# Performance work log

Measured on AMD Instinct MI355X. Metric: run time of the kernel, lower is better.

Reference implementation:

```python
import jax, jax.numpy as jnp
import numpy as np

DELTA = 0.1
PAD = 2  # kernel_size // 2


def _step(x, W):
    # circular padding then VALID 5x5 cross-correlation (matches torch Conv2d circular)
    xp = jnp.pad(x, ((0, 0), (0, 0), (PAD, PAD), (PAD, PAD)), mode='wrap')
    y = jax.lax.conv_general_dilated(
        xp, W, window_strides=(1, 1), padding='VALID',
        dimension_numbers=('NCHW', 'OIHW', 'NCHW'))
    return jnp.clip(x + DELTA * jax.nn.relu(y), 0.0, 1.0)


def setup_inputs() -> dict:
    key = jax.random.key(0)
    k1, k2 = jax.random.split(key)
    x = jax.random.uniform(k1, (16, 3, 1024, 1024), dtype=jnp.float32)
    W = jax.random.normal(k2, (3, 3, 5, 5), dtype=jnp.float32) * 0.2
    return {"x": x, "W": W, "steps": 10}


def reference(x, W, steps):
    for _ in range(steps):
        x = _step(x, W)
    return x
```

## Files before the change

### kernel.cpp

```cpp
#include <hip/hip_runtime.h>


#define HH 1024
#define WW 1024
#define CC 3
#define NB 16
#define TW 128
#define TH 16
#define LW 132
#define LH 20
#define DELTA 0.1f

__global__ __launch_bounds__(256)
void ca_step(const float* __restrict__ src, float* __restrict__ dst,
             const float* __restrict__ Wg) {
    __shared__ float tile[CC][LH][LW];
    __shared__ float wsm[CC * 5 * 16];

    const int tid = threadIdx.x;
    const int w0 = blockIdx.x * TW;
    const int h0 = blockIdx.y * TH;
    const int n  = blockIdx.z;
    const float* srcn = src + (size_t)n * CC * HH * WW;

    if (tid < CC * CC * 25) {
        int oc = tid / 75;
        int rem = tid - oc * 75;
        int ic = rem / 25;
        int r2 = rem - ic * 25;
        int kh = r2 / 5;
        int kw = r2 - kh * 5;
        wsm[(ic * 5 + kh) * 16 + oc * 5 + kw] = Wg[tid];
    }

    for (int f = tid; f < CC * LH * 32; f += 256) {
        int c   = f / (LH * 32);
        int rem = f - c * (LH * 32);
        int row = rem >> 5;
        int c4  = rem & 31;
        int gh = (h0 + row - 2) & (HH - 1);
        const float4 v = *(const float4*)&srcn[((size_t)c * HH + gh) * WW + w0 + 4 * c4];
        float* t = &tile[c][row][2 + 4 * c4];
        *(float2*)&t[0] = make_float2(v.x, v.y);
        *(float2*)&t[2] = make_float2(v.z, v.w);
    }
    if (tid < CC * LH * 2) {
        int side = tid & 1;
        int rf   = tid >> 1;
        int c    = rf / LH;
        int row  = rf - c * LH;
        int gh = (h0 + row - 2) & (HH - 1);
        int gw = side ? ((w0 + TW) & (WW - 1)) : ((w0 - 2) & (WW - 1));
        const float2 v = *(const float2*)&srcn[((size_t)c * HH + gh) * WW + gw];
        *(float2*)&tile[c][row][side ? (2 + TW) : 0] = v;
    }
    __syncthreads();

    const int tx = tid & 31;
    const int ty = tid >> 5;
    const int xb = 4 * tx;

    float acc[2][CC][4];
#pragma unroll
    for (int rg = 0; rg < 2; ++rg)
#pragma unroll
        for (int oc = 0; oc < CC; ++oc)
#pragma unroll
            for (int j = 0; j < 4; ++j) acc[rg][oc][j] = 0.f;
    float xv[2][CC][4];

#pragma unroll
    for (int ic = 0; ic < CC; ++ic) {
#pragma unroll
        for (int kh = 0; kh < 5; ++kh) {
            const float* wrow = &wsm[(ic * 5 + kh) * 16];
            const float4 wA = *(const float4*)&wrow[0];
            const float4 wB = *(const float4*)&wrow[4];
            const float4 wC = *(const float4*)&wrow[8];
            const float4 wD = *(const float4*)&wrow[12];
            const float w_[15] = {wA.x, wA.y, wA.z, wA.w,
                                  wB.x, wB.y, wB.z, wB.w,
                                  wC.x, wC.y, wC.z, wC.w,
                                  wD.x, wD.y, wD.z};
            const float* ra = &tile[ic][ty + kh][xb];
            const float* rb = &tile[ic][ty + 8 + kh][xb];
            float va[8], vb[8];
            *(float4*)&va[0] = *(const float4*)&ra[0];
            *(float4*)&va[4] = *(const float4*)&ra[4];
            *(float4*)&vb[0] = *(const float4*)&rb[0];
            *(float4*)&vb[4] = *(const float4*)&rb[4];
            if (kh == 2) {
#pragma unroll
                for (int j = 0; j < 4; ++j) {
                    xv[0][ic][j] = va[2 + j];
                    xv[1][ic][j] = vb[2 + j];
                }
            }
#pragma unroll
            for (int oc = 0; oc < CC; ++oc) {
#pragma unroll
                for (int kw = 0; kw < 5; ++kw) {
                    const float wv = w_[oc * 5 + kw];
#pragma unroll
                    for (int j = 0; j < 4; ++j) {
                        acc[0][oc][j] = fmaf(va[kw + j], wv, acc[0][oc][j]);
                        acc[1][oc][j] = fmaf(vb[kw + j], wv, acc[1][oc][j]);
                    }
                }
            }
        }
    }

    float* dstn = dst + (size_t)n * CC * HH * WW;
#pragma unroll
    for (int rg = 0; rg < 2; ++rg) {
        const int h = h0 + ty + rg * 8;
#pragma unroll
        for (int oc = 0; oc < CC; ++oc) {
            float4 o;
            o.x = fminf(fmaxf(xv[rg][oc][0] + DELTA * fmaxf(acc[rg][oc][0], 0.f), 0.f), 1.f);
            o.y = fminf(fmaxf(xv[rg][oc][1] + DELTA * fmaxf(acc[rg][oc][1], 0.f), 0.f), 1.f);
            o.z = fminf(fmaxf(xv[rg][oc][2] + DELTA * fmaxf(acc[rg][oc][2], 0.f), 0.f), 1.f);
            o.w = fminf(fmaxf(xv[rg][oc][3] + DELTA * fmaxf(acc[rg][oc][3], 0.f), 0.f), 1.f);
            *(float4*)&dstn[((size_t)oc * HH + h) * WW + w0 + xb] = o;
        }
    }
}

extern "C" void kernel_launch(void* const* d_in, const int* in_sizes, int n_in,
                              void* d_out, int out_size, void* d_ws, size_t ws_size,
                              hipStream_t stream) {
    (void)in_sizes; (void)n_in; (void)out_size;
    const float* x  = (const float*)d_in[0];
    const float* Wg = (const float*)d_in[1];
    const int STEPS = 10;
    float* out = (float*)d_out;
    const size_t buf_bytes = (size_t)NB * CC * HH * WW * sizeof(float);

    dim3 grid(WW / TW, HH / TH, NB);
    dim3 block(256);

    if (ws_size >= buf_bytes) {
        float* tmp = (float*)d_ws;
        const float* s = x;
        for (int i = 1; i <= STEPS; ++i) {
            float* d = (i & 1) ? tmp : out;
            ca_step<<<grid, block, 0, stream>>>(s, d, Wg);
            s = d;
        }
    } else {
        float* tmp = (float*)d_in[0];
        const float* s = x;
        for (int i = 1; i <= STEPS; ++i) {
            float* d = (i & 1) ? out : tmp;
            ca_step<<<grid, block, 0, stream>>>(s, d, Wg);
            s = d;
        }
        hipMemcpyAsync(out, tmp, buf_bytes, hipMemcpyDeviceToDevice, stream);
    }
}
```

Baseline: 1.512 ms.

## Register-block four output rows per thread with rolling row buffer

The block shrinks to 128 threads and each thread now computes four consecutive output rows. Input rows are kept in a rotating four-row register buffer, so each shared-memory row is loaded once per thread instead of once per filter tap row. Weights are read straight from global memory (uniform loads) instead of being staged in shared memory, and the residual x is reread from the tile at the end. This cuts LDS traffic per FMA, at the cost of higher register pressure, fewer threads per tile, and scalar global weight loads inside the inner loop.

```diff
diff --git a/kernel.cpp b/kernel.cpp
--- a/kernel.cpp
+++ b/kernel.cpp
@@ -11,11 +11,10 @@
 #define LH 20
 #define DELTA 0.1f
 
-__global__ __launch_bounds__(256)
+__global__ __launch_bounds__(128, 3)
 void ca_step(const float* __restrict__ src, float* __restrict__ dst,
              const float* __restrict__ Wg) {
     __shared__ float tile[CC][LH][LW];
-    __shared__ float wsm[CC * 5 * 16];
 
     const int tid = threadIdx.x;
     const int w0 = blockIdx.x * TW;
@@ -23,106 +22,95 @@
     const int n  = blockIdx.z;
     const float* srcn = src + (size_t)n * CC * HH * WW;
 
-    if (tid < CC * CC * 25) {
-        int oc = tid / 75;
-        int rem = tid - oc * 75;
-        int ic = rem / 25;
-        int r2 = rem - ic * 25;
-        int kh = r2 / 5;
-        int kw = r2 - kh * 5;
-        wsm[(ic * 5 + kh) * 16 + oc * 5 + kw] = Wg[tid];
-    }
-
-    for (int f = tid; f < CC * LH * 32; f += 256) {
-        int c   = f / (LH * 32);
-        int rem = f - c * (LH * 32);
-        int row = rem >> 5;
-        int c4  = rem & 31;
-        int gh = (h0 + row - 2) & (HH - 1);
+    const int r0 = tid >> 5;
+    const int c4 = tid & 31;
+#pragma unroll
+    for (int k = 0; k < 15; ++k) {
+        const int c     = k / 5;
+        const int strip = k - c * 5;
+        const int row   = strip * 4 + r0;
+        const int gh = (h0 + row - 2) & (HH - 1);
         const float4 v = *(const float4*)&srcn[((size_t)c * HH + gh) * WW + w0 + 4 * c4];
         float* t = &tile[c][row][2 + 4 * c4];
         *(float2*)&t[0] = make_float2(v.x, v.y);
         *(float2*)&t[2] = make_float2(v.z, v.w);
     }
     if (tid < CC * LH * 2) {
-        int side = tid & 1;
-        int rf   = tid >> 1;
-        int c    = rf / LH;
-        int row  = rf - c * LH;
-        int gh = (h0 + row - 2) & (HH - 1);
-        int gw = side ? ((w0 + TW) & (WW - 1)) : ((w0 - 2) & (WW - 1));
+        const int side = tid & 1;
+        const int rf   = tid >> 1;
+        const int c    = rf / LH;
+        const int row  = rf - c * LH;
+        const int gh = (h0 + row - 2) & (HH - 1);
+        const int gw = side ? ((w0 + TW) & (WW - 1)) : ((w0 - 2) & (WW - 1));
         const float2 v = *(const float2*)&srcn[((size_t)c * HH + gh) * WW + gw];
         *(float2*)&tile[c][row][side ? (2 + TW) : 0] = v;
     }
     __syncthreads();
 
-    const int tx = tid & 31;
-    const int ty = tid >> 5;
-    const int xb = 4 * tx;
+    const int tx  = tid & 31;
+    const int ty4 = (tid >> 5) << 2;
+    const int xb  = 4 * tx;
 
-    float acc[2][CC][4];
+    float acc[4][CC][4];
 #pragma unroll
-    for (int rg = 0; rg < 2; ++rg)
+    for (int o = 0; o < 4; ++o)
 #pragma unroll
         for (int oc = 0; oc < CC; ++oc)
 #pragma unroll
-            for (int j = 0; j < 4; ++j) acc[rg][oc][j] = 0.f;
-    float xv[2][CC][4];
+            for (int j = 0; j < 4; ++j) acc[o][oc][j] = 0.f;
 
 #pragma unroll
     for (int ic = 0; ic < CC; ++ic) {
+        float rw[4][8];
+#pragma unroll
+        for (int r = 0; r < 4; ++r) {
+            const float* rp = &tile[ic][ty4 + r][xb];
+            *(float4*)&rw[r][0] = *(const float4*)&rp[0];
+            *(float4*)&rw[r][4] = *(const float4*)&rp[4];
+        }
 #pragma unroll
         for (int kh = 0; kh < 5; ++kh) {
-            const float* wrow = &wsm[(ic * 5 + kh) * 16];
-            const float4 wA = *(const float4*)&wrow[0];
-            const float4 wB = *(const float4*)&wrow[4];
-            const float4 wC = *(const float4*)&wrow[8];
-            const float4 wD = *(const float4*)&wrow[12];
-            const float w_[15] = {wA.x, wA.y, wA.z, wA.w,
-                                  wB.x, wB.y, wB.z, wB.w,
-                                  wC.x, wC.y, wC.z, wC.w,
-                                  wD.x, wD.y, wD.z};
-            const float* ra = &tile[ic][ty + kh][xb];
-            const float* rb = &tile[ic][ty + 8 + kh][xb];
-            float va[8], vb[8];
-            *(float4*)&va[0] = *(const float4*)&ra[0];
-            *(float4*)&va[4] = *(const float4*)&ra[4];
-            *(float4*)&vb[0] = *(const float4*)&rb[0];
-            *(float4*)&vb[4] = *(const float4*)&rb[4];
-            if (kh == 2) {
+            float wsc[CC][5];
 #pragma unroll
-                for (int j = 0; j < 4; ++j) {
-                    xv[0][ic][j] = va[2 + j];
-                    xv[1][ic][j] = vb[2 + j];
-                }
+            for (int oc = 0; oc < CC; ++oc)
+#pragma unroll
+                for (int kw = 0; kw < 5; ++kw)
+                    wsc[oc][kw] = Wg[((oc * CC + ic) * 5 + kh) * 5 + kw];
+#pragma unroll
+            for (int o = 0; o < 4; ++o) {
+#pragma unroll
+                for (int oc = 0; oc < CC; ++oc)
+#pragma unroll
+                    for (int kw = 0; kw < 5; ++kw) {
+                        const float wv = wsc[oc][kw];
+#pragma unroll
+                        for (int j = 0; j < 4; ++j)
+                            acc[o][oc][j] =
+                                fmaf(rw[(kh + o) & 3][kw + j], wv, acc[o][oc][j]);
+                    }
             }
-#pragma unroll
-            for (int oc = 0; oc < CC; ++oc) {
-#pragma unroll
-                for (int kw = 0; kw < 5; ++kw) {
-                    const float wv = w_[oc * 5 + kw];
-#pragma unroll
-                    for (int j = 0; j < 4; ++j) {
-                        acc[0][oc][j] = fmaf(va[kw + j], wv, acc[0][oc][j]);
-                        acc[1][oc][j] = fmaf(vb[kw + j], wv, acc[1][oc][j]);
-                    }
-                }
+            if (kh < 4) {
+                const float* rp = &tile[ic][ty4 + kh + 4][xb];
+                *(float4*)&rw[kh & 3][0] = *(const float4*)&rp[0];
+                *(float4*)&rw[kh & 3][4] = *(const float4*)&rp[4];
             }
         }
     }
 
     float* dstn = dst + (size_t)n * CC * HH * WW;
 #pragma unroll
-    for (int rg = 0; rg < 2; ++rg) {
-        const int h = h0 + ty + rg * 8;
+    for (int o = 0; o < 4; ++o) {
+        const int h = h0 + ty4 + o;
 #pragma unroll
         for (int oc = 0; oc < CC; ++oc) {
-            float4 o;
-            o.x = fminf(fmaxf(xv[rg][oc][0] + DELTA * fmaxf(acc[rg][oc][0], 0.f), 0.f), 1.f);
-            o.y = fminf(fmaxf(xv[rg][oc][1] + DELTA * fmaxf(acc[rg][oc][1], 0.f), 0.f), 1.f);
-            o.z = fminf(fmaxf(xv[rg][oc][2] + DELTA * fmaxf(acc[rg][oc][2], 0.f), 0.f), 1.f);
-            o.w = fminf(fmaxf(xv[rg][oc][3] + DELTA * fmaxf(acc[rg][oc][3], 0.f), 0.f), 1.f);
-            *(float4*)&dstn[((size_t)oc * HH + h) * WW + w0 + xb] = o;
+            const float2 xlo = *(const float2*)&tile[oc][ty4 + o + 2][xb + 2];
+            const float2 xhi = *(const float2*)&tile[oc][ty4 + o + 2][xb + 4];
+            float4 out;
+            out.x = fminf(fmaxf(xlo.x + DELTA * fmaxf(acc[o][oc][0], 0.f), 0.f), 1.f);
+            out.y = fminf(fmaxf(xlo.y + DELTA * fmaxf(acc[o][oc][1], 0.f), 0.f), 1.f);
+            out.z = fminf(fmaxf(xhi.x + DELTA * fmaxf(acc[o][oc][2], 0.f), 0.f), 1.f);
+            out.w = fminf(fmaxf(xhi.y + DELTA * fmaxf(acc[o][oc][3], 0.f), 0.f), 1.f);
+            *(float4*)&dstn[((size_t)oc * HH + h) * WW + w0 + xb] = out;
         }
     }
 }
@@ -138,7 +126,7 @@
     const size_t buf_bytes = (size_t)NB * CC * HH * WW * sizeof(float);
 
     dim3 grid(WW / TW, HH / TH, NB);
-    dim3 block(256);
+    dim3 block(128);
 
     if (ws_size >= buf_bytes) {
         float* tmp = (float*)d_ws;
```

Result: slower. 2.038 ms (+34.8%).

## Assign adjacent row pairs per thread with rolling LDS row buffer and scalar weight loads

Applied to the files above, without the earlier changes.

Each thread now computes two adjacent output rows instead of rows 8 apart. For each of the 5 kernel rows it keeps a rolling two-row register buffer, so each LDS row is read once and shared across both outputs. Weights now come straight from global memory at uniform addresses, which should become scalar loads, instead of being staged through shared memory. Launch bounds now request 5 blocks per CU. The risks are more register pressure, and the ping-pong buffer indexing may not resolve to static registers.

```diff
diff --git a/kernel.cpp b/kernel.cpp
--- a/kernel.cpp
+++ b/kernel.cpp
@@ -11,27 +11,16 @@
 #define LH 20
 #define DELTA 0.1f
 
-__global__ __launch_bounds__(256)
+__global__ __launch_bounds__(256, 5)
 void ca_step(const float* __restrict__ src, float* __restrict__ dst,
              const float* __restrict__ Wg) {
     __shared__ float tile[CC][LH][LW];
-    __shared__ float wsm[CC * 5 * 16];
 
     const int tid = threadIdx.x;
     const int w0 = blockIdx.x * TW;
     const int h0 = blockIdx.y * TH;
     const int n  = blockIdx.z;
     const float* srcn = src + (size_t)n * CC * HH * WW;
-
-    if (tid < CC * CC * 25) {
-        int oc = tid / 75;
-        int rem = tid - oc * 75;
-        int ic = rem / 25;
-        int r2 = rem - ic * 25;
-        int kh = r2 / 5;
-        int kw = r2 - kh * 5;
-        wsm[(ic * 5 + kh) * 16 + oc * 5 + kw] = Wg[tid];
-    }
 
     for (int f = tid; f < CC * LH * 32; f += 256) {
         int c   = f / (LH * 32);
@@ -56,9 +45,9 @@
     }
     __syncthreads();
 
-    const int tx = tid & 31;
-    const int ty = tid >> 5;
-    const int xb = 4 * tx;
+    const int tx  = tid & 31;
+    const int ty2 = (tid >> 5) * 2;
+    const int xb  = 4 * tx;
 
     float acc[2][CC][4];
 #pragma unroll
@@ -71,24 +60,20 @@
 
 #pragma unroll
     for (int ic = 0; ic < CC; ++ic) {
+        float wA[8], wB[8];
+        {
+            const float* ra = &tile[ic][ty2][xb];
+            const float* rb = &tile[ic][ty2 + 1][xb];
+            *(float4*)&wA[0] = *(const float4*)&ra[0];
+            *(float4*)&wA[4] = *(const float4*)&ra[4];
+            *(float4*)&wB[0] = *(const float4*)&rb[0];
+            *(float4*)&wB[4] = *(const float4*)&rb[4];
+        }
 #pragma unroll
         for (int kh = 0; kh < 5; ++kh) {
-            const float* wrow = &wsm[(ic * 5 + kh) * 16];
-            const float4 wA = *(const float4*)&wrow[0];
-            const float4 wB = *(const float4*)&wrow[4];
-            const float4 wC = *(const float4*)&wrow[8];
-            const float4 wD = *(const float4*)&wrow[12];
-            const float w_[15] = {wA.x, wA.y, wA.z, wA.w,
-                                  wB.x, wB.y, wB.z, wB.w,
-                                  wC.x, wC.y, wC.z, wC.w,
-                                  wD.x, wD.y, wD.z};
-            const float* ra = &tile[ic][ty + kh][xb];
-            const float* rb = &tile[ic][ty + 8 + kh][xb];
-            float va[8], vb[8];
-            *(float4*)&va[0] = *(const float4*)&ra[0];
-            *(float4*)&va[4] = *(const float4*)&ra[4];
-            *(float4*)&vb[0] = *(const float4*)&rb[0];
-            *(float4*)&vb[4] = *(const float4*)&rb[4];
+            const float* va = (kh & 1) ? wB : wA;
+            const float* vb = (kh & 1) ? wA : wB;
+
             if (kh == 2) {
 #pragma unroll
                 for (int j = 0; j < 4; ++j) {
@@ -100,7 +85,7 @@
             for (int oc = 0; oc < CC; ++oc) {
 #pragma unroll
                 for (int kw = 0; kw < 5; ++kw) {
-                    const float wv = w_[oc * 5 + kw];
+                    const float wv = Wg[((oc * CC + ic) * 5 + kh) * 5 + kw];
 #pragma unroll
                     for (int j = 0; j < 4; ++j) {
                         acc[0][oc][j] = fmaf(va[kw + j], wv, acc[0][oc][j]);
@@ -108,13 +93,19 @@
                     }
                 }
             }
+            if (kh < 4) {
+                const float* rn = &tile[ic][ty2 + kh + 2][xb];
+                float* wdst = (kh & 1) ? wB : wA;
+                *(float4*)&wdst[0] = *(const float4*)&rn[0];
+                *(float4*)&wdst[4] = *(const float4*)&rn[4];
+            }
         }
     }
 
     float* dstn = dst + (size_t)n * CC * HH * WW;
 #pragma unroll
     for (int rg = 0; rg < 2; ++rg) {
-        const int h = h0 + ty + rg * 8;
+        const int h = h0 + ty2 + rg;
 #pragma unroll
         for (int oc = 0; oc < CC; ++oc) {
             float4 o;
```

Result: slower. 2.642 ms (+74.8%).
